# Performance work log

Hardware: AMD Instinct MI355X
Metric: run time of the kernel (lower is better)

Reference implementation:

```python
import jax, jax.numpy as jnp
import numpy as np

N, M = 8192, 1024
EPS = 1e-6

def _ln(x, g, b):
    mu = jnp.mean(x, axis=-1, keepdims=True)
    var = jnp.mean((x - mu) ** 2, axis=-1, keepdims=True)
    return (x - mu) * jax.lax.rsqrt(var + EPS) * g + b

def setup_inputs() -> dict:
    key = jax.random.key(0)
    ks = jax.random.split(key, 10)
    s = 0.02
    return {
        "x": jax.random.normal(ks[0], (1, N, M), jnp.float32),
        "seq_len": N,
        "Wq": jax.random.normal(ks[1], (M, M), jnp.float32) * s,
        "Wk": jax.random.normal(ks[2], (M, M), jnp.float32) * s,
        "Wv": jax.random.normal(ks[3], (M, M), jnp.float32) * s,
        "Wo": jax.random.normal(ks[4], (M, M), jnp.float32) * s,
        "fc1_w": jax.random.normal(ks[5], (M, M), jnp.float32) * s,
        "fc1_b": jnp.zeros((M,), jnp.float32),
        "ka_w": jax.random.normal(ks[6], (M, M), jnp.float32) * s,
        "ka_b": jnp.zeros((M,), jnp.float32),
        "kd_w": jax.random.normal(ks[7], (1, M), jnp.float32) * s,
        "kd_b": jnp.zeros((1,), jnp.float32),
        "ln_y_g": jnp.ones((M,), jnp.float32),
        "ln_y_b": jnp.zeros((M,), jnp.float32),
        "ln_ka_g": jnp.ones((M,), jnp.float32),
        "ln_ka_b": jnp.zeros((M,), jnp.float32),
    }

def reference(x, seq_len, Wq, Wk, Wv, Wo, fc1_w, fc1_b, ka_w, ka_b, kd_w, kd_b,
              ln_y_g, ln_y_b, ln_ka_g, ln_ka_b):
    xf = x.reshape(-1, M)                      # [n, 1024]
    n = xf.shape[0]
    # ---- DAM (vectorized diff-MLP; dropout = identity in eval) ----
    base = xf[: n - 4]
    d1 = jnp.abs(xf[1 : n - 3] - base)
    d2 = jnp.abs(xf[2 : n - 2] - base)
    d3 = jnp.abs(xf[4 : n] - base)
    fc1 = lambda z: jax.nn.relu(z @ fc1_w.T + fc1_b)
    t = fc1(d1) + fc1(d2) + fc1(d3)            # [n-4, 1024]
    mn = jnp.concatenate([t, xf[n - 4 :]], axis=0)  # [n, 1024]
    # ---- SelfAttention (no masking: apperture=-1, ignore_itself=False) ----
    K = xf @ Wk.T
    Q = (xf @ Wq.T) * 0.06
    V = xf @ Wv.T
    logits = Q @ K.T                           # [n, n]
    aw = jax.nn.softmax(logits, axis=-1)
    # original: y = (V^T @ weights)^T == weights^T @ V
    y = aw.T @ V
    y = y @ Wo.T
    # ---- tail ----
    y = _ln(y + mn, ln_y_g, ln_y_b)
    y = jax.nn.relu(y @ ka_w.T + ka_b)
    y = _ln(y, ln_ka_g, ln_ka_b)
    out = jax.nn.sigmoid(y @ kd_w.T + kd_b)    # [n, 1]
    return out.reshape(1, -1), aw
```

## Files before the change

### kernel.cpp

```cpp
#include <hip/hip_runtime.h>
#include <cstdint>
#include <cstddef>

typedef unsigned short u16;
typedef short bf16x8 __attribute__((ext_vector_type(8)));
typedef float f32x4 __attribute__((ext_vector_type(4)));

#define LN_EPS 1e-6f

#define GLD16(gsrc, ldst) \
    __builtin_amdgcn_global_load_lds( \
        (const __attribute__((address_space(1))) void*)(gsrc), \
        (__attribute__((address_space(3))) void*)(ldst), 16, 0, 0)

__device__ inline u16 f2bf(float f) {
    uint32_t x = __float_as_uint(f);
    uint32_t r = (x + 0x7fffu + ((x >> 16) & 1u)) >> 16;
    return (u16)r;
}
__device__ inline float bf2f(u16 u) { return __uint_as_float(((uint32_t)u) << 16); }

__device__ inline float blk_sum(float v, float* s) {
    #pragma unroll
    for (int o = 32; o > 0; o >>= 1) v += __shfl_xor(v, o);
    __syncthreads();
    if ((threadIdx.x & 63) == 0) s[threadIdx.x >> 6] = v;
    __syncthreads();
    return s[0] + s[1] + s[2] + s[3];
}
__device__ inline float blk_max(float v, float* s) {
    #pragma unroll
    for (int o = 32; o > 0; o >>= 1) v = fmaxf(v, __shfl_xor(v, o));
    __syncthreads();
    if ((threadIdx.x & 63) == 0) s[threadIdx.x >> 6] = v;
    __syncthreads();
    return fmaxf(fmaxf(s[0], s[1]), fmaxf(s[2], s[3]));
}

template<int BN, int MODE>
__global__ __launch_bounds__(512, 2) void gemm8_k(
    const u16* __restrict__ A, int lda, const u16* __restrict__ B, int ldb,
    float* __restrict__ Cf, u16* __restrict__ Cb,
    const float* __restrict__ bias, int ldc, int K, size_t zCstride, float scale)
{
    constexpr int NFRAG = BN / 64;
    constexpr int BKH   = BN * 32;
    constexpr int BUFE  = 16384 + BN * 64;
    __shared__ u16 lds[2 * BUFE];

    const int tid  = threadIdx.x;
    const int lane = tid & 63, wid = tid >> 6;
    const int wr = wid >> 2, wc = wid & 3;
    const int fr = lane & 15, fg = lane >> 4;

    const int gx  = gridDim.x, nwg = gx * gridDim.y;
    const int bid = blockIdx.y * gx + blockIdx.x;
    const int wg  = (bid & 7) * (nwg >> 3) + (bid >> 3);
    const int n0  = (wg % gx) * BN, m0 = (wg / gx) * 256;

    const u16* Az = A + (size_t)blockIdx.z * K;
    const u16* Bz = B + (size_t)blockIdx.z * K;
    float* Cfz = Cf ? Cf + (size_t)blockIdx.z * zCstride : nullptr;

    const int sr = tid >> 2;
    const int kb = ((tid & 3) ^ ((sr >> 1) & 3)) * 8;

    f32x4 acc[8][NFRAG];
    {
        f32x4 z = {0.f, 0.f, 0.f, 0.f};
        #pragma unroll
        for (int m = 0; m < 8; m++)
            #pragma unroll
            for (int n = 0; n < NFRAG; n++) acc[m][n] = z;
    }

    const int NT = K >> 6;

    auto STAGE = [&](int buf, int isB, int kh, int kt) {
        const u16* s0 = isB ? Bz : Az;
        const int  ld = isB ? ldb : lda;
        const int  rb = isB ? n0 : m0;
        const int  k0 = kt * 64 + kh * 32 + kb;
        u16* dst = &lds[buf * BUFE + (isB ? 16384 : 0) + kh * (isB ? BKH : 8192) + tid * 8];
        GLD16(s0 + (size_t)(rb + sr) * ld + k0, dst);
        if (!isB || BN == 256)
            GLD16(s0 + (size_t)(rb + 128 + sr) * ld + k0, dst + 4096);
    };

    #define CKPT_MID() do { if constexpr (BN == 256) asm volatile("s_waitcnt vmcnt(4)" ::: "memory"); \
                            else                     asm volatile("s_waitcnt vmcnt(3)" ::: "memory"); } while (0)

    const int swz   = (fg ^ ((fr >> 1) & 3)) * 8;
    const int baseA = (wr * 128 + fr) * 32 + swz;
    const int baseB = 16384 + (wc * (BN / 4) + fr) * 32 + swz;

    STAGE(0, 0, 0, 0); STAGE(0, 1, 0, 0); STAGE(0, 0, 1, 0); STAGE(0, 1, 1, 0);
    CKPT_MID();
    __builtin_amdgcn_s_barrier();

    bf16x8 af[4], bv[NFRAG];

    for (int t = 0; t < NT; ++t) {
        const int  aO  = (t & 1) * BUFE;
        const int  nxt = (t & 1) ^ 1;
        const bool pre = (t + 1 < NT);

        #pragma unroll
        for (int m = 0; m < 4; m++) af[m] = *(const bf16x8*)&lds[baseA + aO + m * 512];
        #pragma unroll
        for (int n = 0; n < NFRAG; n++) bv[n] = *(const bf16x8*)&lds[baseB + aO + n * 512];
        if (pre) STAGE(nxt, 0, 0, t + 1);
        __builtin_amdgcn_s_barrier();
        asm volatile("s_waitcnt lgkmcnt(0)" ::: "memory");
        __builtin_amdgcn_sched_barrier(0);
        __builtin_amdgcn_s_setprio(1);
        #pragma unroll
        for (int m = 0; m < 4; m++)
            #pragma unroll
            for (int n = 0; n < NFRAG; n++)
                acc[m][n] = __builtin_amdgcn_mfma_f32_16x16x32_bf16(af[m], bv[n], acc[m][n], 0, 0, 0);
        __builtin_amdgcn_s_setprio(0);
        __builtin_amdgcn_s_barrier();

        #pragma unroll
        for (int m = 0; m < 4; m++) af[m] = *(const bf16x8*)&lds[baseA + aO + (4 + m) * 512];
        if (pre) STAGE(nxt, 1, 0, t + 1);
        __builtin_amdgcn_s_barrier();
        asm volatile("s_waitcnt lgkmcnt(0)" ::: "memory");
        __builtin_amdgcn_sched_barrier(0);
        __builtin_amdgcn_s_setprio(1);
        #pragma unroll
        for (int m = 0; m < 4; m++)
            #pragma unroll
            for (int n = 0; n < NFRAG; n++)
                acc[4 + m][n] = __builtin_amdgcn_mfma_f32_16x16x32_bf16(af[m], bv[n], acc[4 + m][n], 0, 0, 0);
        __builtin_amdgcn_s_setprio(0);
        if (pre) { CKPT_MID(); }
        else     { asm volatile("s_waitcnt vmcnt(0)" ::: "memory"); }
        __builtin_amdgcn_sched_barrier(0);
        __builtin_amdgcn_s_barrier();

        #pragma unroll
        for (int m = 0; m < 4; m++) af[m] = *(const bf16x8*)&lds[baseA + aO + 8192 + m * 512];
        #pragma unroll
        for (int n = 0; n < NFRAG; n++) bv[n] = *(const bf16x8*)&lds[baseB + aO + BKH + n * 512];
        if (pre) STAGE(nxt, 0, 1, t + 1);
        __builtin_amdgcn_s_barrier();
        asm volatile("s_waitcnt lgkmcnt(0)" ::: "memory");
        __builtin_amdgcn_sched_barrier(0);
        __builtin_amdgcn_s_setprio(1);
        #pragma unroll
        for (int m = 0; m < 4; m++)
            #pragma unroll
            for (int n = 0; n < NFRAG; n++)
                acc[m][n] = __builtin_amdgcn_mfma_f32_16x16x32_bf16(af[m], bv[n], acc[m][n], 0, 0, 0);
        __builtin_amdgcn_s_setprio(0);
        __builtin_amdgcn_s_barrier();

        #pragma unroll
        for (int m = 0; m < 4; m++) af[m] = *(const bf16x8*)&lds[baseA + aO + 8192 + (4 + m) * 512];
        if (pre) STAGE(nxt, 1, 1, t + 1);
        __builtin_amdgcn_s_barrier();
        asm volatile("s_waitcnt lgkmcnt(0)" ::: "memory");
        __builtin_amdgcn_sched_barrier(0);
        __builtin_amdgcn_s_setprio(1);
        #pragma unroll
        for (int m = 0; m < 4; m++)
            #pragma unroll
            for (int n = 0; n < NFRAG; n++)
                acc[4 + m][n] = __builtin_amdgcn_mfma_f32_16x16x32_bf16(af[m], bv[n], acc[4 + m][n], 0, 0, 0);
        __builtin_amdgcn_s_setprio(0);
        if (pre) { CKPT_MID(); }
        __builtin_amdgcn_sched_barrier(0);
        __builtin_amdgcn_s_barrier();
    }
    #undef CKPT_MID

    #pragma unroll
    for (int m = 0; m < 8; m++)
        #pragma unroll
        for (int n = 0; n < NFRAG; n++)
            #pragma unroll
            for (int r = 0; r < 4; r++) {
                int row = m0 + wr * 128 + m * 16 + fg * 4 + r;
                int col = n0 + wc * (BN / 4) + n * 16 + fr;
                size_t idx = (size_t)row * ldc + col;
                float v = acc[m][n][r] * scale;
                if (MODE == 0) {
                    Cfz[idx] = v;
                } else if (MODE == 1) {
                    Cfz[idx] = fmaxf(v + bias[col], 0.f);
                } else if (MODE == 2) {
                    Cfz[idx] += fmaxf(v + bias[col], 0.f);
                } else {
                    Cb[idx] = f2bf(v);
                }
            }
}

__global__ __launch_bounds__(256) void cvt_k(const float* __restrict__ s, u16* __restrict__ d) {
    int i = blockIdx.x * 256 + threadIdx.x;
    const float4* sf = reinterpret_cast<const float4*>(s);
    float4 a = sf[2 * i], b = sf[2 * i + 1];
    union { u16 u[8]; int4 v; } t;
    t.u[0] = f2bf(a.x); t.u[1] = f2bf(a.y); t.u[2] = f2bf(a.z); t.u[3] = f2bf(a.w);
    t.u[4] = f2bf(b.x); t.u[5] = f2bf(b.y); t.u[6] = f2bf(b.z); t.u[7] = f2bf(b.w);
    reinterpret_cast<int4*>(d)[i] = t.v;
}

__global__ __launch_bounds__(256) void cvt6_k(
    const float* __restrict__ s0, const float* __restrict__ s1, const float* __restrict__ s2,
    const float* __restrict__ s3, const float* __restrict__ s4, const float* __restrict__ s5,
    u16* __restrict__ d0, u16* __restrict__ d1, u16* __restrict__ d2,
    u16* __restrict__ d3, u16* __restrict__ d4, u16* __restrict__ d5) {
    int w = blockIdx.x >> 9;
    const float* s = (w == 0) ? s0 : (w == 1) ? s1 : (w == 2) ? s2 : (w == 3) ? s3 : (w == 4) ? s4 : s5;
    u16*         d = (w == 0) ? d0 : (w == 1) ? d1 : (w == 2) ? d2 : (w == 3) ? d3 : (w == 4) ? d4 : d5;
    int i = (blockIdx.x & 511) * 256 + threadIdx.x;
    const float4* sf = reinterpret_cast<const float4*>(s);
    float4 a = sf[2 * i], b = sf[2 * i + 1];
    union { u16 u[8]; int4 v; } t;
    t.u[0] = f2bf(a.x); t.u[1] = f2bf(a.y); t.u[2] = f2bf(a.z); t.u[3] = f2bf(a.w);
    t.u[4] = f2bf(b.x); t.u[5] = f2bf(b.y); t.u[6] = f2bf(b.z); t.u[7] = f2bf(b.w);
    reinterpret_cast<int4*>(d)[i] = t.v;
}

__global__ __launch_bounds__(256) void cvt2_k(const float* __restrict__ s0, const float* __restrict__ s1,
                                              u16* __restrict__ d) {
    int i = blockIdx.x * 256 + threadIdx.x;
    const float4* f0 = reinterpret_cast<const float4*>(s0);
    const float4* f1 = reinterpret_cast<const float4*>(s1);
    float4 a = f0[2 * i], b = f0[2 * i + 1];
    float4 c = f1[2 * i], e = f1[2 * i + 1];
    union { u16 u[8]; int4 v; } t;
    t.u[0] = f2bf(a.x + c.x); t.u[1] = f2bf(a.y + c.y);
    t.u[2] = f2bf(a.z + c.z); t.u[3] = f2bf(a.w + c.w);
    t.u[4] = f2bf(b.x + e.x); t.u[5] = f2bf(b.y + e.y);
    t.u[6] = f2bf(b.z + e.z); t.u[7] = f2bf(b.w + e.w);
    reinterpret_cast<int4*>(d)[i] = t.v;
}

__global__ __launch_bounds__(256) void diff3_k(const float* __restrict__ x,
                                               u16* __restrict__ d1, u16* __restrict__ d2,
                                               u16* __restrict__ d3) {
    int i4 = blockIdx.x * 256 + threadIdx.x;
    int row = i4 >> 8;
    const float4* xf = reinterpret_cast<const float4*>(x);
    ushort4 o1, o2, o3;
    if (row < 8188) {
        float4 b  = xf[i4];
        float4 a1 = xf[i4 + (1 << 8)];
        float4 a2 = xf[i4 + (2 << 8)];
        float4 a3 = xf[i4 + (4 << 8)];
        o1.x = f2bf(fabsf(a1.x - b.x)); o1.y = f2bf(fabsf(a1.y - b.y));
        o1.z = f2bf(fabsf(a1.z - b.z)); o1.w = f2bf(fabsf(a1.w - b.w));
        o2.x = f2bf(fabsf(a2.x - b.x)); o2.y = f2bf(fabsf(a2.y - b.y));
        o2.z = f2bf(fabsf(a2.z - b.z)); o2.w = f2bf(fabsf(a2.w - b.w));
        o3.x = f2bf(fabsf(a3.x - b.x)); o3.y = f2bf(fabsf(a3.y - b.y));
        o3.z = f2bf(fabsf(a3.z - b.z)); o3.w = f2bf(fabsf(a3.w - b.w));
    } else {
        o1.x = o1.y = o1.z = o1.w = 0;
        o2 = o1; o3 = o1;
    }
    reinterpret_cast<ushort4*>(d1)[i4] = o1;
    reinterpret_cast<ushort4*>(d2)[i4] = o2;
    reinterpret_cast<ushort4*>(d3)[i4] = o3;
}

__global__ __launch_bounds__(256) void tail_k(const float* __restrict__ x, float* __restrict__ mn) {
    int i = blockIdx.x * 256 + threadIdx.x;
    mn[8188 * 1024 + i] = x[8188 * 1024 + i];
}

__global__ __launch_bounds__(256) void softmax_k(const float* __restrict__ S,
                                                 float* __restrict__ aw, int row0) {
    __shared__ float red[4];
    int r = blockIdx.x, tid = threadIdx.x;
    const float4* src = reinterpret_cast<const float4*>(S + (size_t)r * 8192);
    float4 xv[8];
    float mx = -1e30f;
    #pragma unroll
    for (int j = 0; j < 8; j++) {
        xv[j] = src[tid + 256 * j];
        mx = fmaxf(mx, fmaxf(fmaxf(xv[j].x, xv[j].y), fmaxf(xv[j].z, xv[j].w)));
    }
    mx = blk_max(mx, red);
    float sum = 0.f;
    #pragma unroll
    for (int j = 0; j < 8; j++) {
        xv[j].x = __expf(xv[j].x - mx); sum += xv[j].x;
        xv[j].y = __expf(xv[j].y - mx); sum += xv[j].y;
        xv[j].z = __expf(xv[j].z - mx); sum += xv[j].z;
        xv[j].w = __expf(xv[j].w - mx); sum += xv[j].w;
    }
    sum = blk_sum(sum, red);
    float inv = 1.0f / sum;
    float4* dst = reinterpret_cast<float4*>(aw + (size_t)(row0 + r) * 8192);
    #pragma unroll
    for (int j = 0; j < 8; j++) {
        float4 o;
        o.x = xv[j].x * inv; o.y = xv[j].y * inv; o.z = xv[j].z * inv; o.w = xv[j].w * inv;
        dst[tid + 256 * j] = o;
    }
}

__global__ __launch_bounds__(256) void transpose_f32_bf16(const float* __restrict__ src,
                                                          u16* __restrict__ dst) {
    __shared__ u16 t[64][72];
    int r0 = blockIdx.y * 64, c0 = blockIdx.x * 64;
    int tid = threadIdx.x;
    #pragma unroll
    for (int p = 0; p < 4; p++) {
        int q = p * 256 + tid;
        int r = q >> 4, c4 = q & 15;
        float4 v = *(reinterpret_cast<const float4*>(src + (size_t)(r0 + r) * 8192 + c0) + c4);
        t[c4 * 4 + 0][r] = f2bf(v.x);
        t[c4 * 4 + 1][r] = f2bf(v.y);
        t[c4 * 4 + 2][r] = f2bf(v.z);
        t[c4 * 4 + 3][r] = f2bf(v.w);
    }
    __syncthreads();
    #pragma unroll
    for (int p = 0; p < 2; p++) {
        int q = p * 256 + tid;
        int rr = q >> 3, cc = q & 7;
        *reinterpret_cast<int4*>(dst + (size_t)(c0 + rr) * 8192 + r0 + cc * 8) =
            *reinterpret_cast<const int4*>(&t[rr][cc * 8]);
    }
}

__global__ __launch_bounds__(256) void transpose_bf16(const u16* __restrict__ src,
                                                      u16* __restrict__ dst,
                                                      int srcld, int dstld) {
    __shared__ u16 t[64][72];
    int r0 = blockIdx.y * 64, c0 = blockIdx.x * 64;
    int tid = threadIdx.x;
    #pragma unroll
    for (int p = 0; p < 2; p++) {
        int q = p * 256 + tid;
        int r = q >> 3, c8 = q & 7;
        int4 v = *(reinterpret_cast<const int4*>(src + (size_t)(r0 + r) * srcld + c0) + c8);
        const u16* u = reinterpret_cast<const u16*>(&v);
        #pragma unroll
        for (int k = 0; k < 8; k++) t[c8 * 8 + k][r] = u[k];
    }
    __syncthreads();
    #pragma unroll
    for (int p = 0; p < 2; p++) {
        int q = p * 256 + tid;
        int rr = q >> 3, cc = q & 7;
        *reinterpret_cast<int4*>(dst + (size_t)(c0 + rr) * dstld + r0 + cc * 8) =
            *reinterpret_cast<const int4*>(&t[rr][cc * 8]);
    }
}

__global__ __launch_bounds__(256) void ln_y_k(const float* __restrict__ y2, const float* __restrict__ mn,
                                              const float* __restrict__ g, const float* __restrict__ b,
                                              u16* __restrict__ zb) {
    __shared__ float red[4];
    int r = blockIdx.x, tid = threadIdx.x;
    float4 a = reinterpret_cast<const float4*>(y2 + (size_t)r * 1024)[tid];
    float4 c = reinterpret_cast<const float4*>(mn + (size_t)r * 1024)[tid];
    float4 v; v.x = a.x + c.x; v.y = a.y + c.y; v.z = a.z + c.z; v.w = a.w + c.w;
    float s  = v.x + v.y + v.z + v.w;
    float sq = v.x * v.x + v.y * v.y + v.z * v.z + v.w * v.w;
    s  = blk_sum(s, red);
    sq = blk_sum(sq, red);
    float mu = s * (1.0f / 1024.0f);
    float rs = rsqrtf(sq * (1.0f / 1024.0f) - mu * mu + LN_EPS);
    float4 gg = reinterpret_cast<const float4*>(g)[tid];
    float4 bb = reinterpret_cast<const float4*>(b)[tid];
    ushort4 o;
    o.x = f2bf((v.x - mu) * rs * gg.x + bb.x);
    o.y = f2bf((v.y - mu) * rs * gg.y + bb.y);
    o.z = f2bf((v.z - mu) * rs * gg.z + bb.z);
    o.w = f2bf((v.w - mu) * rs * gg.w + bb.w);
    reinterpret_cast<ushort4*>(zb + (size_t)r * 1024)[tid] = o;
}

__global__ __launch_bounds__(256) void ln_dot_k(const float* __restrict__ h, const float* __restrict__ g,
                                                const float* __restrict__ b, const float* __restrict__ kd,
                                                const float* __restrict__ kdb, float* __restrict__ out) {
    __shared__ float red[4];
    int r = blockIdx.x, tid = threadIdx.x;
    float4 v = reinterpret_cast<const float4*>(h + (size_t)r * 1024)[tid];
    float s  = v.x + v.y + v.z + v.w;
    float sq = v.x * v.x + v.y * v.y + v.z * v.z + v.w * v.w;
    s  = blk_sum(s, red);
    sq = blk_sum(sq, red);
    float mu = s * (1.0f / 1024.0f);
    float rs = rsqrtf(sq * (1.0f / 1024.0f) - mu * mu + LN_EPS);
    float4 gg = reinterpret_cast<const float4*>(g)[tid];
    float4 bb = reinterpret_cast<const float4*>(b)[tid];
    float4 kk = reinterpret_cast<const float4*>(kd)[tid];
    float part = ((v.x - mu) * rs * gg.x + bb.x) * kk.x
               + ((v.y - mu) * rs * gg.y + bb.y) * kk.y
               + ((v.z - mu) * rs * gg.z + bb.z) * kk.z
               + ((v.w - mu) * rs * gg.w + bb.w) * kk.w;
    part = blk_sum(part, red);
    if (tid == 0) out[r] = 1.0f / (1.0f + __expf(-(part + kdb[0])));
}

extern "C" void kernel_launch(void* const* d_in, const int* in_sizes, int n_in,
                              void* d_out, int out_size, void* d_ws, size_t ws_size,
                              hipStream_t stream) {
    (void)in_sizes; (void)n_in; (void)out_size; (void)ws_size;
    const float* x    = (const float*)d_in[0];
    const float* Wq   = (const float*)d_in[2];
    const float* Wk   = (const float*)d_in[3];
    const float* Wv   = (const float*)d_in[4];
    const float* Wo   = (const float*)d_in[5];
    const float* fc1w = (const float*)d_in[6];
    const float* fc1b = (const float*)d_in[7];
    const float* kaw  = (const float*)d_in[8];
    const float* kab  = (const float*)d_in[9];
    const float* kdw  = (const float*)d_in[10];
    const float* kdb  = (const float*)d_in[11];
    const float* lyg  = (const float*)d_in[12];
    const float* lyb  = (const float*)d_in[13];
    const float* lkg  = (const float*)d_in[14];
    const float* lkb  = (const float*)d_in[15];

    float* out0 = (float*)d_out;
    float* aw   = out0 + 8192;

    char* base = (char*)d_ws;
    size_t off = 0;
    auto alloc = [&](size_t bytes) -> char* {
        char* p = base + off;
        off += (bytes + 255) & ~(size_t)255;
        return p;
    };
    const size_t NM = 8192ULL * 1024ULL;
    u16*   ST   = (u16*)alloc(8192ULL * 8192ULL * 2);
    float* Sf   = (float*)ST;
    u16*   xb   = (u16*)alloc(NM * 2);
    u16*   Qb   = (u16*)alloc(NM * 2);
    u16*   Kb   = (u16*)alloc(NM * 2);
    u16*   Vb   = (u16*)alloc(NM * 2);
    u16*   Vt   = (u16*)alloc(NM * 2);
    u16*   d1   = (u16*)alloc(NM * 2);
    u16*   d2   = (u16*)alloc(NM * 2);
    u16*   d3   = (u16*)alloc(NM * 2);
    u16*   yb   = (u16*)alloc(NM * 2);
    float* mn   = (float*)alloc(NM * 4);
    float* y01  = (float*)alloc(NM * 4 * 2);
    float* y2   = (float*)alloc(NM * 4);
    float* hbuf = (float*)alloc(NM * 4);
    u16*   Wqb  = (u16*)alloc(1048576ULL * 2);
    u16*   Wkb  = (u16*)alloc(1048576ULL * 2);
    u16*   Wvb  = (u16*)alloc(1048576ULL * 2);
    u16*   fwb  = (u16*)alloc(1048576ULL * 2);
    u16*   Wob  = (u16*)alloc(1048576ULL * 2);
    u16*   kwb  = (u16*)alloc(1048576ULL * 2);
    u16*   zb   = d1;

    cvt_k<<<4096, 256, 0, stream>>>(x, xb);
    cvt6_k<<<3072, 256, 0, stream>>>(Wq, Wk, Wv, fc1w, Wo, kaw,
                                     Wqb, Wkb, Wvb, fwb, Wob, kwb);

    diff3_k<<<8192, 256, 0, stream>>>(x, d1, d2, d3);
    gemm8_k<128, 1><<<dim3(8, 32), 512, 0, stream>>>(
        d1, 1024, fwb, 1024, mn, nullptr, fc1b, 1024, 1024, 0, 1.0f);
    gemm8_k<128, 2><<<dim3(8, 32), 512, 0, stream>>>(
        d2, 1024, fwb, 1024, mn, nullptr, fc1b, 1024, 1024, 0, 1.0f);
    gemm8_k<128, 2><<<dim3(8, 32), 512, 0, stream>>>(
        d3, 1024, fwb, 1024, mn, nullptr, fc1b, 1024, 1024, 0, 1.0f);
    tail_k<<<16, 256, 0, stream>>>(x, mn);

    gemm8_k<128, 3><<<dim3(8, 32), 512, 0, stream>>>(
        xb, 1024, Wqb, 1024, nullptr, Qb, nullptr, 1024, 1024, 0, 0.06f);
    gemm8_k<128, 3><<<dim3(8, 32), 512, 0, stream>>>(
        xb, 1024, Wkb, 1024, nullptr, Kb, nullptr, 1024, 1024, 0, 1.0f);
    gemm8_k<128, 3><<<dim3(8, 32), 512, 0, stream>>>(
        xb, 1024, Wvb, 1024, nullptr, Vb, nullptr, 1024, 1024, 0, 1.0f);
    transpose_bf16<<<dim3(16, 128), 256, 0, stream>>>(Vb, Vt, 1024, 8192);

    for (int c = 0; c < 2; ++c) {
        gemm8_k<256, 0><<<dim3(32, 16), 512, 0, stream>>>(
            Qb + (size_t)c * 4096 * 1024, 1024, Kb, 1024,
            Sf, nullptr, nullptr, 8192, 1024, 0, 1.0f);
        softmax_k<<<4096, 256, 0, stream>>>(Sf, aw, c * 4096);
    }

    transpose_f32_bf16<<<dim3(128, 128), 256, 0, stream>>>(aw, ST);
    gemm8_k<256, 0><<<dim3(4, 32, 2), 512, 0, stream>>>(
        ST, 8192, Vt, 8192, y01, nullptr, nullptr, 1024, 4096, NM, 1.0f);
    cvt2_k<<<4096, 256, 0, stream>>>(y01, y01 + NM, yb);

    gemm8_k<128, 0><<<dim3(8, 32), 512, 0, stream>>>(
        yb, 1024, Wob, 1024, y2, nullptr, nullptr, 1024, 1024, 0, 1.0f);
    ln_y_k<<<8192, 256, 0, stream>>>(y2, mn, lyg, lyb, zb);
    gemm8_k<128, 1><<<dim3(8, 32), 512, 0, stream>>>(
        zb, 1024, kwb, 1024, hbuf, nullptr, kab, 1024, 1024, 0, 1.0f);
    ln_dot_k<<<8192, 256, 0, stream>>>(hbuf, lkg, lkb, kdw, kdb, out0);
}
```

Measured before the change: 784.5 us.

## Fuse softmax normalization into transpose and fold x bf16 conversion into diff kernel

Softmax is split into a row-statistics kernel (max and inverse sum) and a combined normalize-and-transpose kernel. That kernel writes the fp32 attention weights and the transposed bf16 copy in one pass, so the later re-read of the full attention matrix is gone. The x-to-bf16 conversion is merged into the diff kernel, which already loads x. The cost is a second read of the score buffer, and scores need their own workspace instead of aliasing the transpose buffer.

New measurement: 775.7 us. No clear change (-1.1%).

```diff
diff --git a/kernel.cpp b/kernel.cpp
--- a/kernel.cpp
+++ b/kernel.cpp
@@ -198,16 +198,6 @@
             }
 }
 
-__global__ __launch_bounds__(256) void cvt_k(const float* __restrict__ s, u16* __restrict__ d) {
-    int i = blockIdx.x * 256 + threadIdx.x;
-    const float4* sf = reinterpret_cast<const float4*>(s);
-    float4 a = sf[2 * i], b = sf[2 * i + 1];
-    union { u16 u[8]; int4 v; } t;
-    t.u[0] = f2bf(a.x); t.u[1] = f2bf(a.y); t.u[2] = f2bf(a.z); t.u[3] = f2bf(a.w);
-    t.u[4] = f2bf(b.x); t.u[5] = f2bf(b.y); t.u[6] = f2bf(b.z); t.u[7] = f2bf(b.w);
-    reinterpret_cast<int4*>(d)[i] = t.v;
-}
-
 __global__ __launch_bounds__(256) void cvt6_k(
     const float* __restrict__ s0, const float* __restrict__ s1, const float* __restrict__ s2,
     const float* __restrict__ s3, const float* __restrict__ s4, const float* __restrict__ s5,
@@ -240,15 +230,18 @@
     reinterpret_cast<int4*>(d)[i] = t.v;
 }
 
-__global__ __launch_bounds__(256) void diff3_k(const float* __restrict__ x,
-                                               u16* __restrict__ d1, u16* __restrict__ d2,
-                                               u16* __restrict__ d3) {
+__global__ __launch_bounds__(256) void diff3x_k(const float* __restrict__ x,
+                                                u16* __restrict__ d1, u16* __restrict__ d2,
+                                                u16* __restrict__ d3, u16* __restrict__ xb) {
     int i4 = blockIdx.x * 256 + threadIdx.x;
     int row = i4 >> 8;
     const float4* xf = reinterpret_cast<const float4*>(x);
+    float4 b = xf[i4];
+    ushort4 ox;
+    ox.x = f2bf(b.x); ox.y = f2bf(b.y); ox.z = f2bf(b.z); ox.w = f2bf(b.w);
+    reinterpret_cast<ushort4*>(xb)[i4] = ox;
     ushort4 o1, o2, o3;
     if (row < 8188) {
-        float4 b  = xf[i4];
         float4 a1 = xf[i4 + (1 << 8)];
         float4 a2 = xf[i4 + (2 << 8)];
         float4 a3 = xf[i4 + (4 << 8)];
@@ -272,8 +265,8 @@
     mn[8188 * 1024 + i] = x[8188 * 1024 + i];
 }
 
-__global__ __launch_bounds__(256) void softmax_k(const float* __restrict__ S,
-                                                 float* __restrict__ aw, int row0) {
+__global__ __launch_bounds__(256) void stats_k(const float* __restrict__ S,
+                                               float* __restrict__ rowm, float* __restrict__ rowl) {
     __shared__ float red[4];
     int r = blockIdx.x, tid = threadIdx.x;
     const float4* src = reinterpret_cast<const float4*>(S + (size_t)r * 8192);
@@ -288,24 +281,18 @@
     float sum = 0.f;
     #pragma unroll
     for (int j = 0; j < 8; j++) {
-        xv[j].x = __expf(xv[j].x - mx); sum += xv[j].x;
-        xv[j].y = __expf(xv[j].y - mx); sum += xv[j].y;
-        xv[j].z = __expf(xv[j].z - mx); sum += xv[j].z;
-        xv[j].w = __expf(xv[j].w - mx); sum += xv[j].w;
+        sum += __expf(xv[j].x - mx) + __expf(xv[j].y - mx)
+             + __expf(xv[j].z - mx) + __expf(xv[j].w - mx);
     }
     sum = blk_sum(sum, red);
-    float inv = 1.0f / sum;
-    float4* dst = reinterpret_cast<float4*>(aw + (size_t)(row0 + r) * 8192);
-    #pragma unroll
-    for (int j = 0; j < 8; j++) {
-        float4 o;
-        o.x = xv[j].x * inv; o.y = xv[j].y * inv; o.z = xv[j].z * inv; o.w = xv[j].w * inv;
-        dst[tid + 256 * j] = o;
-    }
-}
-
-__global__ __launch_bounds__(256) void transpose_f32_bf16(const float* __restrict__ src,
-                                                          u16* __restrict__ dst) {
+    if (tid == 0) { rowm[r] = mx; rowl[r] = 1.0f / sum; }
+}
+
+__global__ __launch_bounds__(256) void nt_k(const float* __restrict__ Sf,
+                                            const float* __restrict__ rowm,
+                                            const float* __restrict__ rowl,
+                                            float* __restrict__ awc,
+                                            u16* __restrict__ ST, int colbase) {
     __shared__ u16 t[64][72];
     int r0 = blockIdx.y * 64, c0 = blockIdx.x * 64;
     int tid = threadIdx.x;
@@ -313,18 +300,25 @@
     for (int p = 0; p < 4; p++) {
         int q = p * 256 + tid;
         int r = q >> 4, c4 = q & 15;
-        float4 v = *(reinterpret_cast<const float4*>(src + (size_t)(r0 + r) * 8192 + c0) + c4);
-        t[c4 * 4 + 0][r] = f2bf(v.x);
-        t[c4 * 4 + 1][r] = f2bf(v.y);
-        t[c4 * 4 + 2][r] = f2bf(v.z);
-        t[c4 * 4 + 3][r] = f2bf(v.w);
+        float4 v = *(reinterpret_cast<const float4*>(Sf + (size_t)(r0 + r) * 8192 + c0) + c4);
+        float m  = rowm[r0 + r], li = rowl[r0 + r];
+        float4 o;
+        o.x = __expf(v.x - m) * li;
+        o.y = __expf(v.y - m) * li;
+        o.z = __expf(v.z - m) * li;
+        o.w = __expf(v.w - m) * li;
+        *(reinterpret_cast<float4*>(awc + (size_t)(r0 + r) * 8192 + c0) + c4) = o;
+        t[c4 * 4 + 0][r] = f2bf(o.x);
+        t[c4 * 4 + 1][r] = f2bf(o.y);
+        t[c4 * 4 + 2][r] = f2bf(o.z);
+        t[c4 * 4 + 3][r] = f2bf(o.w);
     }
     __syncthreads();
     #pragma unroll
     for (int p = 0; p < 2; p++) {
         int q = p * 256 + tid;
         int rr = q >> 3, cc = q & 7;
-        *reinterpret_cast<int4*>(dst + (size_t)(c0 + rr) * 8192 + r0 + cc * 8) =
+        *reinterpret_cast<int4*>(ST + (size_t)(c0 + rr) * 8192 + colbase + r0 + cc * 8) =
             *reinterpret_cast<const int4*>(&t[rr][cc * 8]);
     }
 }
@@ -433,7 +427,7 @@
     };
     const size_t NM = 8192ULL * 1024ULL;
     u16*   ST   = (u16*)alloc(8192ULL * 8192ULL * 2);
-    float* Sf   = (float*)ST;
+    float* Sf   = (float*)alloc(4096ULL * 8192ULL * 4);
     u16*   xb   = (u16*)alloc(NM * 2);
     u16*   Qb   = (u16*)alloc(NM * 2);
     u16*   Kb   = (u16*)alloc(NM * 2);
@@ -453,13 +447,14 @@
     u16*   fwb  = (u16*)alloc(1048576ULL * 2);
     u16*   Wob  = (u16*)alloc(1048576ULL * 2);
     u16*   kwb  = (u16*)alloc(1048576ULL * 2);
+    float* rowm = (float*)alloc(4096ULL * 4);
+    float* rowl = (float*)alloc(4096ULL * 4);
     u16*   zb   = d1;
 
-    cvt_k<<<4096, 256, 0, stream>>>(x, xb);
+    diff3x_k<<<8192, 256, 0, stream>>>(x, d1, d2, d3, xb);
     cvt6_k<<<3072, 256, 0, stream>>>(Wq, Wk, Wv, fc1w, Wo, kaw,
                                      Wqb, Wkb, Wvb, fwb, Wob, kwb);
 
-    diff3_k<<<8192, 256, 0, stream>>>(x, d1, d2, d3);
     gemm8_k<128, 1><<<dim3(8, 32), 512, 0, stream>>>(
         d1, 1024, fwb, 1024, mn, nullptr, fc1b, 1024, 1024, 0, 1.0f);
     gemm8_k<128, 2><<<dim3(8, 32), 512, 0, stream>>>(
@@ -480,10 +475,11 @@
         gemm8_k<256, 0><<<dim3(32, 16), 512, 0, stream>>>(
             Qb + (size_t)c * 4096 * 1024, 1024, Kb, 1024,
             Sf, nullptr, nullptr, 8192, 1024, 0, 1.0f);
-        softmax_k<<<4096, 256, 0, stream>>>(Sf, aw, c * 4096);
-    }
-
-    transpose_f32_bf16<<<dim3(128, 128), 256, 0, stream>>>(aw, ST);
+        stats_k<<<4096, 256, 0, stream>>>(Sf, rowm, rowl);
+        nt_k<<<dim3(128, 64), 256, 0, stream>>>(Sf, rowm, rowl,
+            aw + (size_t)c * 4096 * 8192, ST, c * 4096);
+    }
+
     gemm8_k<256, 0><<<dim3(4, 32, 2), 512, 0, stream>>>(
         ST, 8192, Vt, 8192, y01, nullptr, nullptr, 1024, 4096, NM, 1.0f);
     cvt2_k<<<4096, 256, 0, stream>>>(y01, y01 + NM, yb);
```
